# Kernel tuning notes

Hardware: AMD Instinct MI355X
Metric: run time of the kernel (lower is better)

## Reference

```python
import jax, jax.numpy as jnp
from jax import lax
import numpy as np

C = 64          # in_channel
CL = 32         # latent channels = in_channel // latent_dim
IC = 32         # inter_channel
GH, GW = 8, 8   # grid


def conv1x1(x, W, b):
    # x: [N,C,H,W], W: [O,C], b: [O]
    return jnp.einsum('nchw,oc->nohw', x, W) + b[None, :, None, None]


def maxpool2(x):
    return lax.reduce_window(x, -jnp.inf, lax.max, (1, 1, 2, 2), (1, 1, 2, 2), 'VALID')


def conv3x3(x, W, b):
    y = lax.conv_general_dilated(x, W, (1, 1), ((1, 1), (1, 1)),
                                 dimension_numbers=('NCHW', 'OIHW', 'NCHW'))
    return y + b[None, :, None, None]


def setup_inputs() -> dict:
    key = jax.random.key(0)
    ks = jax.random.split(key, 20)
    s = 0.05
    inp = {
        'x': jax.random.normal(ks[0], (4, C, 256, 256), jnp.float32),
        # Self_Attn_FM params (1x1 convs stored as matrices)
        'Wq': jax.random.normal(ks[1], (CL, C), jnp.float32) * s,
        'bq': jnp.zeros((CL,), jnp.float32),
        'Wk': jax.random.normal(ks[2], (CL, C), jnp.float32) * s,
        'bk': jnp.zeros((CL,), jnp.float32),
        'Wv': jax.random.normal(ks[3], (CL, C), jnp.float32) * s,
        'bv': jnp.zeros((CL,), jnp.float32),
        'Wo': jax.random.normal(ks[4], (C, CL), jnp.float32) * s,
        'bo': jnp.zeros((C,), jnp.float32),
        'gamma': jax.random.normal(ks[5], ()) * 0.5,
        # dense conv blocks: dims 64 -> 96 -> 128, each -> 32
        'W1': jax.random.normal(ks[6], (IC, C, 3, 3), jnp.float32) * s,
        'b1': jnp.zeros((IC,), jnp.float32),
        'W2': jax.random.normal(ks[7], (IC, C + IC, 3, 3), jnp.float32) * s,
        'b2': jnp.zeros((IC,), jnp.float32),
        'W3': jax.random.normal(ks[8], (IC, C + 2 * IC, 3, 3), jnp.float32) * s,
        'b3': jnp.zeros((IC,), jnp.float32),
        # fusion 1x1: (C + 3*IC) -> C
        'Wf': jax.random.normal(ks[9], (C, C + 3 * IC), jnp.float32) * s,
        'bf': jnp.zeros((C,), jnp.float32),
    }
    return inp


def region_non_local(x, Wq, bq, Wk, bk, Wv, bv, Wo, bo, gamma):
    B, Cc, H, W = x.shape
    h, w = H // GH, W // GW
    # split into grid cells, batched: [B*GH*GW, C, h, w]
    cells = x.reshape(B, Cc, GH, h, GW, w).transpose(0, 2, 4, 1, 3, 5)
    cells = cells.reshape(B * GH * GW, Cc, h, w)
    N, L = cells.shape[0], h * w
    q = conv1x1(cells, Wq, bq).reshape(N, CL, L)                 # [N,c,L]
    k = maxpool2(conv1x1(cells, Wk, bk)).reshape(N, CL, L // 4)  # [N,c,L/4]
    v = maxpool2(conv1x1(cells, Wv, bv)).reshape(N, CL, L // 4)
    attn = jax.nn.softmax(jnp.einsum('ncq,nck->nqk', q, k), axis=-1)
    out = jnp.einsum('nck,nqk->ncq', v, attn).reshape(N, CL, h, w)
    out = gamma * conv1x1(out, Wo, bo) + cells
    # regroup cells back to [B,C,H,W]
    out = out.reshape(B, GH, GW, Cc, h, w).transpose(0, 3, 1, 4, 2, 5)
    return out.reshape(B, Cc, H, W)


def reference(x, Wq, bq, Wk, bk, Wv, bv, Wo, bo, gamma,
              W1, b1, W2, b2, W3, b3, Wf, bf):
    f0 = region_non_local(x, Wq, bq, Wk, bk, Wv, bv, Wo, bo, gamma)
    f1 = jax.nn.relu(conv3x3(f0, W1, b1))
    f2 = jax.nn.relu(conv3x3(jnp.concatenate([f0, f1], axis=1), W2, b2))
    f3 = jax.nn.relu(conv3x3(jnp.concatenate([f0, f1, f2], axis=1), W3, b3))
    cat = jnp.concatenate([f0, f1, f2, f3], axis=1)
    out = conv1x1(cat, Wf, bf) + x
    return out
```

## Files before the change

### kernel.cpp

```cpp
#include <hip/hip_runtime.h>


typedef short s16x8 __attribute__((ext_vector_type(8)));
typedef float f32x4 __attribute__((ext_vector_type(4)));
typedef unsigned short ushort_t;

__device__ __forceinline__ unsigned short f2bf(float f) {
  union { float f; unsigned int u; } v; v.f = f;
  unsigned int r = v.u + 0x7fffu + ((v.u >> 16) & 1u);
  return (unsigned short)(r >> 16);
}
__device__ __forceinline__ float bf2f(unsigned short h) {
  union { unsigned int u; float f; } v; v.u = ((unsigned int)h) << 16;
  return v.f;
}

__global__ void repack_kernel(const float* __restrict__ W1, const float* __restrict__ W2,
                              const float* __restrict__ W3, const float* __restrict__ Wf,
                              ushort_t* __restrict__ wc1, ushort_t* __restrict__ wc2,
                              ushort_t* __restrict__ wc3, ushort_t* __restrict__ wff)
{
  const int i = blockIdx.x * 256 + threadIdx.x;
  if (i < 18432) {
    int j = i & 7, o = (i >> 3) & 31, r = i >> 8, tap = r >> 3, kg = r & 7;
    wc1[i] = f2bf(W1[o * 576 + (kg * 8 + j) * 9 + tap]);
  }
  if (i < 27648) {
    int j = i & 7, o = (i >> 3) & 31, r = i >> 8, tap = r / 12, kg = r % 12;
    wc2[i] = f2bf(W2[o * 864 + (kg * 8 + j) * 9 + tap]);
  }
  if (i < 36864) {
    int j = i & 7, o = (i >> 3) & 31, r = i >> 8, tap = r >> 4, kg = r & 15;
    wc3[i] = f2bf(W3[o * 1152 + (kg * 8 + j) * 9 + tap]);
  }
  if (i < 10240) {
    int j = i & 7, o = (i >> 3) & 63, kg = i >> 9;
    wff[i] = f2bf(Wf[o * 160 + kg * 8 + j]);
  }
}

__global__ __launch_bounds__(256, 4) void kvx_kernel(
    const float* __restrict__ x,
    const float* __restrict__ Wk, const float* __restrict__ bk,
    const float* __restrict__ Wv, const float* __restrict__ bv,
    ushort_t* __restrict__ xt, ushort_t* __restrict__ kg, ushort_t* __restrict__ vt)
{
  __shared__ ushort_t kvs[4][8][64];

  const int bid = blockIdx.x;
  const int cell = bid >> 3;
  const int tid = threadIdx.x, lane = tid & 63, wv = tid >> 6;
  const int w = (bid & 7) * 4 + wv;
  const int yp = w >> 1, h = w & 1;
  const int quad = lane >> 4, l15 = lane & 15;

  const int n  = cell >> 6;
  const int gh = (cell >> 3) & 7;
  const int gw = cell & 7;
  const int y0 = gh * 32, xc0 = gw * 32;
  const float* xn  = x  + (size_t)n * (64 * 65536);
  ushort_t*    xtn = xt + (size_t)n * (65536 * 64);

  s16x8 wkf[2][2], wvf[2][2];
#pragma unroll
  for (int ks = 0; ks < 2; ++ks)
#pragma unroll
    for (int nt = 0; nt < 2; ++nt) {
      const int off = (nt * 16 + l15) * 64 + ks * 32 + quad * 8;
      s16x8 tk, tv;
#pragma unroll
      for (int j = 0; j < 8; ++j) {
        tk[j] = (short)f2bf(Wk[off + j]);
        tv[j] = (short)f2bf(Wv[off + j]);
      }
      wkf[ks][nt] = tk; wvf[ks][nt] = tv;
    }
  float bkv[2], bvv[2];
#pragma unroll
  for (int nt = 0; nt < 2; ++nt) {
    bkv[nt] = bk[nt * 16 + l15];
    bvv[nt] = bv[nt * 16 + l15];
  }

  const f32x4 zf = {0.f, 0.f, 0.f, 0.f};
  f32x4 kd[2][2], vd[2][2];

#pragma unroll
  for (int t2 = 0; t2 < 2; ++t2) {
    const int yy = 2 * yp + t2;
    const int xx = h * 16 + l15;
    const float* px = xn + (y0 + yy) * 256 + xc0 + xx;

    s16x8 a[2];
#pragma unroll
    for (int ks = 0; ks < 2; ++ks)
#pragma unroll
      for (int j = 0; j < 8; ++j)
        a[ks][j] = (short)f2bf(px[(size_t)(ks * 32 + quad * 8 + j) * 65536]);

    const size_t pixg = (size_t)((y0 + yy) * 256 + xc0 + xx);
    *(s16x8*)(xtn + pixg * 64 + quad * 8)      = a[0];
    *(s16x8*)(xtn + pixg * 64 + 32 + quad * 8) = a[1];

#pragma unroll
    for (int nt = 0; nt < 2; ++nt) {
      kd[t2][nt] = zf; vd[t2][nt] = zf;
#pragma unroll
      for (int ks = 0; ks < 2; ++ks) {
        kd[t2][nt] = __builtin_amdgcn_mfma_f32_16x16x32_bf16(a[ks], wkf[ks][nt], kd[t2][nt], 0, 0, 0);
        vd[t2][nt] = __builtin_amdgcn_mfma_f32_16x16x32_bf16(a[ks], wvf[ks][nt], vd[t2][nt], 0, 0, 0);
      }
    }
  }

#pragma unroll
  for (int nt = 0; nt < 2; ++nt) {
#pragma unroll
    for (int r = 0; r < 2; ++r) {
      const float kp = fmaxf(fmaxf(kd[0][nt][2 * r], kd[0][nt][2 * r + 1]),
                             fmaxf(kd[1][nt][2 * r], kd[1][nt][2 * r + 1])) + bkv[nt];
      const float vp = fmaxf(fmaxf(vd[0][nt][2 * r], vd[0][nt][2 * r + 1]),
                             fmaxf(vd[1][nt][2 * r], vd[1][nt][2 * r + 1])) + bvv[nt];
      kvs[wv][quad * 2 + r][nt * 16 + l15]      = f2bf(kp);
      kvs[wv][quad * 2 + r][32 + nt * 16 + l15] = f2bf(vp);
    }
  }
  __syncthreads();

  const int kpos0 = yp * 16 + h * 8;
  if (lane < 32) {
    const s16x8 vv = *(const s16x8*)&kvs[wv][lane >> 2][(lane & 3) * 8];
    *(s16x8*)(kg + ((size_t)(cell << 8) + kpos0 + (lane >> 2)) * 32 + (lane & 3) * 8) = vv;
  } else {
    const int ch = lane - 32;
    s16x8 vv;
#pragma unroll
    for (int r = 0; r < 8; ++r) vv[r] = (short)kvs[wv][r][32 + ch];
    *(s16x8*)(vt + (size_t)(cell << 13) + ch * 256 + kpos0) = vv;
  }
}

__global__ __launch_bounds__(256, 3) void attn_kernel(
    const ushort_t* __restrict__ xt, const ushort_t* __restrict__ kg,
    const ushort_t* __restrict__ vt,
    const float* __restrict__ Wq, const float* __restrict__ bq,
    const float* __restrict__ Wo, const float* __restrict__ bo,
    const float* __restrict__ gamma_p, ushort_t* __restrict__ f0)
{
  __shared__ __attribute__((aligned(16))) ushort_t kl[256 * 36];
  __shared__ __attribute__((aligned(16))) ushort_t vl[32 * 260];
  __shared__ __attribute__((aligned(16))) ushort_t un[4][2176];

  const int bid = blockIdx.x;
  const int cell = bid >> 2;
  const int part = bid & 3;
  const int tid = threadIdx.x, lane = tid & 63, wv = tid >> 6;
  const int quad = lane >> 4, l15 = lane & 15;

  const int n  = cell >> 6;
  const int gh = (cell >> 3) & 7;
  const int gw = cell & 7;
  const int y0 = gh * 32, xc0 = gw * 32;

  const ushort_t* xtn = xt + (size_t)n * (65536 * 64);
  ushort_t*       f0n = f0 + (size_t)n * (65536 * 64);
  const ushort_t* kc  = kg + (size_t)(cell << 8) * 32;
  const ushort_t* vc  = vt + (size_t)(cell << 13);

  for (int idx = tid; idx < 1024; idx += 256) {
    const int kpos = idx >> 2, cg = idx & 3;
    *(s16x8*)&kl[kpos * 36 + cg * 8] = *(const s16x8*)(kc + kpos * 32 + cg * 8);
  }
  for (int idx = tid; idx < 1024; idx += 256) {
    const int ch = idx >> 5, seg = idx & 31;
    *(s16x8*)&vl[ch * 260 + seg * 8] = *(const s16x8*)(vc + ch * 256 + seg * 8);
  }

  const float gamma = gamma_p[0];

  s16x8 wqf[2][2];
#pragma unroll
  for (int ks = 0; ks < 2; ++ks)
#pragma unroll
    for (int nt = 0; nt < 2; ++nt) {
      const float* p = Wq + (nt * 16 + l15) * 64 + ks * 32 + quad * 8;
      s16x8 t;
#pragma unroll
      for (int j = 0; j < 8; ++j) t[j] = (short)f2bf(p[j]);
      wqf[ks][nt] = t;
    }
  s16x8 wof[4];
#pragma unroll
  for (int nt = 0; nt < 4; ++nt) {
    const float* p = Wo + (nt * 16 + l15) * 32 + quad * 8;
    s16x8 t;
#pragma unroll
    for (int j = 0; j < 8; ++j) t[j] = (short)f2bf(p[j]);
    wof[nt] = t;
  }
  float bqv[2]; bqv[0] = bq[l15]; bqv[1] = bq[16 + l15];
  float bov[4];
#pragma unroll
  for (int nt = 0; nt < 4; ++nt) bov[nt] = bo[nt * 16 + l15];

  __syncthreads();

  ushort_t* uw = un[wv];
  const f32x4 zf = {0.f, 0.f, 0.f, 0.f};

#pragma unroll 1
  for (int it = 0; it < 4; ++it) {
    const int mt = part * 16 + wv * 4 + it;
    const int pbase = mt * 16;

    const int p = pbase + l15;
    const int yy = p >> 5, xx = p & 31;
    const size_t pixg = (size_t)((y0 + yy) * 256 + xc0 + xx);

    const s16x8 a0 = *(const s16x8*)(xtn + pixg * 64 + quad * 8);
    const s16x8 a1 = *(const s16x8*)(xtn + pixg * 64 + 32 + quad * 8);
    f32x4 qd0 = zf, qd1 = zf;
    qd0 = __builtin_amdgcn_mfma_f32_16x16x32_bf16(a0, wqf[0][0], qd0, 0, 0, 0);
    qd0 = __builtin_amdgcn_mfma_f32_16x16x32_bf16(a1, wqf[1][0], qd0, 0, 0, 0);
    qd1 = __builtin_amdgcn_mfma_f32_16x16x32_bf16(a0, wqf[0][1], qd1, 0, 0, 0);
    qd1 = __builtin_amdgcn_mfma_f32_16x16x32_bf16(a1, wqf[1][1], qd1, 0, 0, 0);
#pragma unroll
    for (int i = 0; i < 4; ++i) {
      uw[(quad * 4 + i) * 40 + l15]      = f2bf(qd0[i] + bqv[0]);
      uw[(quad * 4 + i) * 40 + 16 + l15] = f2bf(qd1[i] + bqv[1]);
    }
    const s16x8 qa = *(const s16x8*)&uw[l15 * 40 + quad * 8];

    f32x4 S[16];
#pragma unroll
    for (int nt = 0; nt < 16; ++nt) {
      const s16x8 kb = *(const s16x8*)&kl[(nt * 16 + l15) * 36 + quad * 8];
      S[nt] = __builtin_amdgcn_mfma_f32_16x16x32_bf16(qa, kb, zf, 0, 0, 0);
    }

    float rl[4];
#pragma unroll
    for (int i = 0; i < 4; ++i) {
      float m = S[0][i];
#pragma unroll
      for (int nt = 1; nt < 16; ++nt) m = fmaxf(m, S[nt][i]);
#pragma unroll
      for (int d2 = 1; d2 < 16; d2 <<= 1) m = fmaxf(m, __shfl_xor(m, d2, 64));
      float s = 0.f;
#pragma unroll
      for (int nt = 0; nt < 16; ++nt) {
        float e = __expf(S[nt][i] - m);
        S[nt][i] = e;
        s += e;
      }
#pragma unroll
      for (int d2 = 1; d2 < 16; d2 <<= 1) s += __shfl_xor(s, d2, 64);
      rl[i] = s;
    }

    f32x4 O0 = zf, O1 = zf;
#pragma unroll
    for (int hh = 0; hh < 2; ++hh) {
#pragma unroll
      for (int t = 0; t < 8; ++t)
#pragma unroll
        for (int i = 0; i < 4; ++i)
          uw[(quad * 4 + i) * 136 + t * 16 + l15] = f2bf(S[hh * 8 + t][i]);
#pragma unroll
      for (int kk = 0; kk < 4; ++kk) {
        const s16x8 pa = *(const s16x8*)&uw[l15 * 136 + kk * 32 + quad * 8];
        const int kb0 = hh * 128 + kk * 32 + quad * 8;
        const s16x8 vb0 = *(const s16x8*)&vl[l15 * 260 + kb0];
        const s16x8 vb1 = *(const s16x8*)&vl[(16 + l15) * 260 + kb0];
        O0 = __builtin_amdgcn_mfma_f32_16x16x32_bf16(pa, vb0, O0, 0, 0, 0);
        O1 = __builtin_amdgcn_mfma_f32_16x16x32_bf16(pa, vb1, O1, 0, 0, 0);
      }
    }

#pragma unroll
    for (int i = 0; i < 4; ++i) {
      const float inv = 1.0f / rl[i];
      uw[(quad * 4 + i) * 40 + l15]      = f2bf(O0[i] * inv);
      uw[(quad * 4 + i) * 40 + 16 + l15] = f2bf(O1[i] * inv);
    }
    const s16x8 oa = *(const s16x8*)&uw[l15 * 40 + quad * 8];
#pragma unroll
    for (int nt = 0; nt < 4; ++nt) {
      f32x4 D = __builtin_amdgcn_mfma_f32_16x16x32_bf16(oa, wof[nt], zf, 0, 0, 0);
#pragma unroll
      for (int i = 0; i < 4; ++i)
        uw[(quad * 4 + i) * 72 + nt * 16 + l15] = f2bf(gamma * (D[i] + bov[nt]));
    }

    {
      const s16x8 fv0 = *(const s16x8*)&uw[l15 * 72 + quad * 16];
      const s16x8 fv1 = *(const s16x8*)&uw[l15 * 72 + quad * 16 + 8];
      const s16x8 xv0 = *(const s16x8*)(xtn + pixg * 64 + quad * 16);
      const s16x8 xv1 = *(const s16x8*)(xtn + pixg * 64 + quad * 16 + 8);
      s16x8 r0, r1;
#pragma unroll
      for (int j = 0; j < 8; ++j) {
        r0[j] = (short)f2bf(bf2f((unsigned short)fv0[j]) + bf2f((unsigned short)xv0[j]));
        r1[j] = (short)f2bf(bf2f((unsigned short)fv1[j]) + bf2f((unsigned short)xv1[j]));
      }
      *(s16x8*)(f0n + pixg * 64 + quad * 16)     = r0;
      *(s16x8*)(f0n + pixg * 64 + quad * 16 + 8) = r1;
    }
  }
}

template <int NCHUNK>
__global__ __launch_bounds__(256) void conv3_kernel(
    const ushort_t* __restrict__ s0, const ushort_t* __restrict__ s1,
    const ushort_t* __restrict__ s2, const ushort_t* __restrict__ wc,
    const float* __restrict__ bias, ushort_t* __restrict__ outp)
{
  __shared__ __attribute__((aligned(16))) ushort_t tile[612 * 40];

  const int bid = blockIdx.x;
  const int n = bid >> 7;
  const int t = bid & 127;
  const int ty0 = (t >> 3) * 16;
  const int tx0 = (t & 7) * 32;
  const int tid = threadIdx.x, lane = tid & 63, wv = tid >> 6;
  const int quad = lane >> 4, l15 = lane & 15;
  constexpr int Kg = NCHUNK * 4;

  const f32x4 zf = {0.f, 0.f, 0.f, 0.f};
  f32x4 acc[4][2][2];
#pragma unroll
  for (int r = 0; r < 4; ++r)
#pragma unroll
    for (int h = 0; h < 2; ++h) { acc[r][h][0] = zf; acc[r][h][1] = zf; }

  for (int ch = 0; ch < NCHUNK; ++ch) {
    const ushort_t* src; int cstr, cbase;
    if (ch < 2)       { src = s0 + (size_t)n * (65536 * 64); cstr = 64; cbase = ch * 32; }
    else if (ch == 2) { src = s1 + (size_t)n * (65536 * 32); cstr = 32; cbase = 0; }
    else              { src = s2 + (size_t)n * (65536 * 32); cstr = 32; cbase = 0; }

    __syncthreads();
    for (int u = tid; u < 2448; u += 256) {
      const int pix = u >> 2, cg = u & 3;
      const int lr = pix / 34, lc = pix - lr * 34;
      const int gy = ty0 - 1 + lr, gx = tx0 - 1 + lc;
      s16x8 v = {0, 0, 0, 0, 0, 0, 0, 0};
      if ((unsigned)gy < 256u && (unsigned)gx < 256u)
        v = *(const s16x8*)(src + (size_t)(gy * 256 + gx) * cstr + cbase + cg * 8);
      *(s16x8*)&tile[pix * 40 + cg * 8] = v;
    }
    __syncthreads();

#pragma unroll
    for (int tap = 0; tap < 9; ++tap) {
      const int ky = tap / 3, kx = tap - ky * 3;
      const ushort_t* wb = wc + ((size_t)(tap * Kg + ch * 4 + quad) * 32 + l15) * 8;
      const s16x8 b0 = *(const s16x8*)wb;
      const s16x8 b1 = *(const s16x8*)(wb + 128);
#pragma unroll
      for (int r = 0; r < 4; ++r) {
        const int lr = 4 * wv + r + ky;
#pragma unroll
        for (int h = 0; h < 2; ++h) {
          const int lc = h * 16 + l15 + kx;
          const s16x8 a = *(const s16x8*)&tile[(lr * 34 + lc) * 40 + quad * 8];
          acc[r][h][0] = __builtin_amdgcn_mfma_f32_16x16x32_bf16(a, b0, acc[r][h][0], 0, 0, 0);
          acc[r][h][1] = __builtin_amdgcn_mfma_f32_16x16x32_bf16(a, b1, acc[r][h][1], 0, 0, 0);
        }
      }
    }
  }

  const float bv0 = bias[l15], bv1 = bias[16 + l15];
  ushort_t* on = outp + (size_t)n * (65536 * 32);
#pragma unroll
  for (int r = 0; r < 4; ++r) {
    const int gy = ty0 + 4 * wv + r;
#pragma unroll
    for (int h = 0; h < 2; ++h) {
#pragma unroll
      for (int i = 0; i < 4; ++i) {
        const int gx = tx0 + h * 16 + quad * 4 + i;
        ushort_t* op = on + (size_t)(gy * 256 + gx) * 32;
        op[l15]      = f2bf(fmaxf(acc[r][h][0][i] + bv0, 0.f));
        op[16 + l15] = f2bf(fmaxf(acc[r][h][1][i] + bv1, 0.f));
      }
    }
  }
}

__global__ __launch_bounds__(256) void fuse_kernel(
    const ushort_t* __restrict__ f0, const ushort_t* __restrict__ f1,
    const ushort_t* __restrict__ f2, const ushort_t* __restrict__ f3,
    const float* __restrict__ x, const ushort_t* __restrict__ wff,
    const float* __restrict__ bfv, float* __restrict__ out)
{
  __shared__ float tr[4][64 * 17];

  const int tid = threadIdx.x, lane = tid & 63, wv = tid >> 6;
  const int quad = lane >> 4, l15 = lane & 15;

  s16x8 wf[5][4];
#pragma unroll
  for (int ks = 0; ks < 5; ++ks)
#pragma unroll
    for (int nt = 0; nt < 4; ++nt)
      wf[ks][nt] = *(const s16x8*)(wff + ((size_t)((ks * 4 + quad) * 64) + nt * 16 + l15) * 8);
  float bb[4];
#pragma unroll
  for (int nt = 0; nt < 4; ++nt) bb[nt] = bfv[nt * 16 + l15];

  const int wt = blockIdx.x * 4 + wv;
  const f32x4 zf = {0.f, 0.f, 0.f, 0.f};
  float* trw = tr[wv];

  for (int mt = 0; mt < 4; ++mt) {
    const int p0 = wt * 64 + mt * 16;
    const size_t pA = (size_t)(p0 + l15);
    const s16x8 a0 = *(const s16x8*)(f0 + pA * 64 + quad * 8);
    const s16x8 a1 = *(const s16x8*)(f0 + pA * 64 + 32 + quad * 8);
    const s16x8 a2 = *(const s16x8*)(f1 + pA * 32 + quad * 8);
    const s16x8 a3 = *(const s16x8*)(f2 + pA * 32 + quad * 8);
    const s16x8 a4 = *(const s16x8*)(f3 + pA * 32 + quad * 8);

    f32x4 acc[4];
#pragma unroll
    for (int nt = 0; nt < 4; ++nt) {
      f32x4 d = zf;
      d = __builtin_amdgcn_mfma_f32_16x16x32_bf16(a0, wf[0][nt], d, 0, 0, 0);
      d = __builtin_amdgcn_mfma_f32_16x16x32_bf16(a1, wf[1][nt], d, 0, 0, 0);
      d = __builtin_amdgcn_mfma_f32_16x16x32_bf16(a2, wf[2][nt], d, 0, 0, 0);
      d = __builtin_amdgcn_mfma_f32_16x16x32_bf16(a3, wf[3][nt], d, 0, 0, 0);
      d = __builtin_amdgcn_mfma_f32_16x16x32_bf16(a4, wf[4][nt], d, 0, 0, 0);
      acc[nt] = d;
    }

#pragma unroll
    for (int nt = 0; nt < 4; ++nt)
#pragma unroll
      for (int i = 0; i < 4; ++i)
        trw[(nt * 16 + l15) * 17 + quad * 4 + i] = acc[nt][i] + bb[nt];

    const int n = p0 >> 16;
    const int pix0 = p0 & 65535;
    const float* xb = x + (size_t)n * (64 * 65536);
    float* ob = out + (size_t)n * (64 * 65536);
#pragma unroll
    for (int og = 0; og < 16; ++og) {
      const int o = og * 4 + quad;
      const float v = trw[o * 17 + l15];
      const size_t g = (size_t)o * 65536 + pix0 + l15;
      ob[g] = v + xb[g];
    }
  }
}

extern "C" void kernel_launch(void* const* d_in, const int* in_sizes, int n_in,
                              void* d_out, int out_size, void* d_ws, size_t ws_size,
                              hipStream_t stream)
{
  const float* x     = (const float*)d_in[0];
  const float* Wq    = (const float*)d_in[1];
  const float* bq    = (const float*)d_in[2];
  const float* Wk    = (const float*)d_in[3];
  const float* bk    = (const float*)d_in[4];
  const float* Wv    = (const float*)d_in[5];
  const float* bv    = (const float*)d_in[6];
  const float* Wo    = (const float*)d_in[7];
  const float* bo    = (const float*)d_in[8];
  const float* gamma = (const float*)d_in[9];
  const float* W1    = (const float*)d_in[10];
  const float* b1    = (const float*)d_in[11];
  const float* W2    = (const float*)d_in[12];
  const float* b2    = (const float*)d_in[13];
  const float* W3    = (const float*)d_in[14];
  const float* b3    = (const float*)d_in[15];
  const float* Wf    = (const float*)d_in[16];
  const float* bf    = (const float*)d_in[17];

  float* out = (float*)d_out;
  ushort_t* wsu = (ushort_t*)d_ws;

  ushort_t* f0 = wsu;
  ushort_t* f1 = wsu + 16777216;
  ushort_t* f2 = wsu + 25165824;
  ushort_t* f3 = wsu + 33554432;
  ushort_t* xtb = wsu + 16777216;
  ushort_t* kgb = wsu + 33554432;
  ushort_t* vtb = wsu + 35651584;
  ushort_t* wc1 = wsu + 41943040;
  ushort_t* wc2 = wc1 + 18432;
  ushort_t* wc3 = wc2 + 27648;
  ushort_t* wff = wc3 + 36864;

  repack_kernel<<<144, 256, 0, stream>>>(W1, W2, W3, Wf, wc1, wc2, wc3, wff);
  kvx_kernel<<<2048, 256, 0, stream>>>(x, Wk, bk, Wv, bv, xtb, kgb, vtb);
  attn_kernel<<<1024, 256, 0, stream>>>(xtb, kgb, vtb, Wq, bq, Wo, bo, gamma, f0);
  conv3_kernel<2><<<512, 256, 0, stream>>>(f0, f1, f2, wc1, b1, f1);
  conv3_kernel<3><<<512, 256, 0, stream>>>(f0, f1, f2, wc2, b2, f2);
  conv3_kernel<4><<<512, 256, 0, stream>>>(f0, f1, f2, wc3, b3, f3);
  fuse_kernel<<<1024, 256, 0, stream>>>(f0, f1, f2, f3, x, wff, bf, out);
}
```

Measured before the change: 342.5 us.

## Stage x rows through LDS in kvx kernel for coalesced vectorized loads

Each kvx block now covers a 2-row by 128-pixel strip for one image. It loads that strip from x with coalesced float4 reads, converts to bf16 and writes it into a padded LDS tile. The channel-last xt copy and the K/V MFMA inputs are then gathered from LDS, replacing the earlier scattered per-channel global loads with a 65536 stride. The grid is halved and each wave processes two tiles, at the cost of about 33KB of LDS per block and an extra barrier, which may reduce occupancy.

```diff
diff --git a/kernel.cpp b/kernel.cpp
--- a/kernel.cpp
+++ b/kernel.cpp
@@ -45,21 +45,37 @@
     const float* __restrict__ Wv, const float* __restrict__ bv,
     ushort_t* __restrict__ xt, ushort_t* __restrict__ kg, ushort_t* __restrict__ vt)
 {
+  __shared__ __attribute__((aligned(16))) ushort_t lds[64 * 258];
   __shared__ ushort_t kvs[4][8][64];
 
   const int bid = blockIdx.x;
-  const int cell = bid >> 3;
+  const int n   = bid >> 8;
+  const int rem = bid & 255;
+  const int pr  = rem >> 1;
+  const int xh  = rem & 1;
   const int tid = threadIdx.x, lane = tid & 63, wv = tid >> 6;
-  const int w = (bid & 7) * 4 + wv;
-  const int yp = w >> 1, h = w & 1;
   const int quad = lane >> 4, l15 = lane & 15;
 
-  const int n  = cell >> 6;
-  const int gh = (cell >> 3) & 7;
-  const int gw = cell & 7;
-  const int y0 = gh * 32, xc0 = gw * 32;
-  const float* xn  = x  + (size_t)n * (64 * 65536);
-  ushort_t*    xtn = xt + (size_t)n * (65536 * 64);
+  const int y0 = pr * 2;
+  const int x0 = xh * 128;
+  const int gh = pr >> 4, pyc = pr & 15;
+
+  const float* xblk = x + (size_t)n * (64 * 65536) + (size_t)(y0 * 256 + x0);
+  ushort_t*    xtn  = xt + (size_t)n * (65536 * 64);
+
+#pragma unroll 4
+  for (int i = 0; i < 16; ++i) {
+    const int idx = (i << 8) + tid;
+    const int c  = idx >> 6;
+    const int r  = (idx >> 5) & 1;
+    const int sg = idx & 31;
+    const f32x4 v = *(const f32x4*)(xblk + (size_t)c * 65536 + r * 256 + sg * 4);
+    const unsigned int lo = (unsigned int)f2bf(v[0]) | ((unsigned int)f2bf(v[1]) << 16);
+    const unsigned int hi = (unsigned int)f2bf(v[2]) | ((unsigned int)f2bf(v[3]) << 16);
+    const int base = c * 258 + (r << 7) + (sg << 2);
+    *(unsigned int*)&lds[base]     = lo;
+    *(unsigned int*)&lds[base + 2] = hi;
+  }
 
   s16x8 wkf[2][2], wvf[2][2];
 #pragma unroll
@@ -82,61 +98,76 @@
     bvv[nt] = bv[nt * 16 + l15];
   }
 
+  __syncthreads();
+
+  {
+    const int g  = lane & 7;
+    const int pa = lane >> 3;
+#pragma unroll
+    for (int s = 0; s < 8; ++s) {
+      const int p = (wv << 6) + (s << 3) + pa;
+      s16x8 v;
+#pragma unroll
+      for (int j = 0; j < 8; ++j) v[j] = (short)lds[(g * 8 + j) * 258 + p];
+      const int P = (y0 + (p >> 7)) * 256 + x0 + (p & 127);
+      *(s16x8*)(xtn + (size_t)P * 64 + g * 8) = v;
+    }
+  }
+
   const f32x4 zf = {0.f, 0.f, 0.f, 0.f};
-  f32x4 kd[2][2], vd[2][2];
-
-#pragma unroll
-  for (int t2 = 0; t2 < 2; ++t2) {
-    const int yy = 2 * yp + t2;
-    const int xx = h * 16 + l15;
-    const float* px = xn + (y0 + yy) * 256 + xc0 + xx;
-
-    s16x8 a[2];
-#pragma unroll
-    for (int ks = 0; ks < 2; ++ks)
-#pragma unroll
-      for (int j = 0; j < 8; ++j)
-        a[ks][j] = (short)f2bf(px[(size_t)(ks * 32 + quad * 8 + j) * 65536]);
-
-    const size_t pixg = (size_t)((y0 + yy) * 256 + xc0 + xx);
-    *(s16x8*)(xtn + pixg * 64 + quad * 8)      = a[0];
-    *(s16x8*)(xtn + pixg * 64 + 32 + quad * 8) = a[1];
-
-#pragma unroll
-    for (int nt = 0; nt < 2; ++nt) {
-      kd[t2][nt] = zf; vd[t2][nt] = zf;
+#pragma unroll
+  for (int tt = 0; tt < 2; ++tt) {
+    const int t   = wv * 2 + tt;
+    const int px0 = t * 16 + l15;
+
+    s16x8 a[2][2];
+#pragma unroll
+    for (int r = 0; r < 2; ++r)
 #pragma unroll
       for (int ks = 0; ks < 2; ++ks) {
-        kd[t2][nt] = __builtin_amdgcn_mfma_f32_16x16x32_bf16(a[ks], wkf[ks][nt], kd[t2][nt], 0, 0, 0);
-        vd[t2][nt] = __builtin_amdgcn_mfma_f32_16x16x32_bf16(a[ks], wvf[ks][nt], vd[t2][nt], 0, 0, 0);
-      }
-    }
-  }
-
-#pragma unroll
-  for (int nt = 0; nt < 2; ++nt) {
-#pragma unroll
-    for (int r = 0; r < 2; ++r) {
-      const float kp = fmaxf(fmaxf(kd[0][nt][2 * r], kd[0][nt][2 * r + 1]),
-                             fmaxf(kd[1][nt][2 * r], kd[1][nt][2 * r + 1])) + bkv[nt];
-      const float vp = fmaxf(fmaxf(vd[0][nt][2 * r], vd[0][nt][2 * r + 1]),
-                             fmaxf(vd[1][nt][2 * r], vd[1][nt][2 * r + 1])) + bvv[nt];
-      kvs[wv][quad * 2 + r][nt * 16 + l15]      = f2bf(kp);
-      kvs[wv][quad * 2 + r][32 + nt * 16 + l15] = f2bf(vp);
-    }
-  }
-  __syncthreads();
-
-  const int kpos0 = yp * 16 + h * 8;
-  if (lane < 32) {
-    const s16x8 vv = *(const s16x8*)&kvs[wv][lane >> 2][(lane & 3) * 8];
-    *(s16x8*)(kg + ((size_t)(cell << 8) + kpos0 + (lane >> 2)) * 32 + (lane & 3) * 8) = vv;
-  } else {
-    const int ch = lane - 32;
-    s16x8 vv;
-#pragma unroll
-    for (int r = 0; r < 8; ++r) vv[r] = (short)kvs[wv][r][32 + ch];
-    *(s16x8*)(vt + (size_t)(cell << 13) + ch * 256 + kpos0) = vv;
+        s16x8 v;
+#pragma unroll
+        for (int j = 0; j < 8; ++j)
+          v[j] = (short)lds[(ks * 32 + quad * 8 + j) * 258 + (r << 7) + px0];
+        a[r][ks] = v;
+      }
+
+    f32x4 kd[2][2], vd[2][2];
+#pragma unroll
+    for (int r = 0; r < 2; ++r)
+#pragma unroll
+      for (int nt = 0; nt < 2; ++nt) {
+        f32x4 k0 = __builtin_amdgcn_mfma_f32_16x16x32_bf16(a[r][0], wkf[0][nt], zf, 0, 0, 0);
+        kd[r][nt] = __builtin_amdgcn_mfma_f32_16x16x32_bf16(a[r][1], wkf[1][nt], k0, 0, 0, 0);
+        f32x4 v0 = __builtin_amdgcn_mfma_f32_16x16x32_bf16(a[r][0], wvf[0][nt], zf, 0, 0, 0);
+        vd[r][nt] = __builtin_amdgcn_mfma_f32_16x16x32_bf16(a[r][1], wvf[1][nt], v0, 0, 0, 0);
+      }
+
+#pragma unroll
+    for (int nt = 0; nt < 2; ++nt)
+#pragma unroll
+      for (int rr = 0; rr < 2; ++rr) {
+        const float kp = fmaxf(fmaxf(kd[0][nt][2 * rr], kd[0][nt][2 * rr + 1]),
+                               fmaxf(kd[1][nt][2 * rr], kd[1][nt][2 * rr + 1])) + bkv[nt];
+        const float vp = fmaxf(fmaxf(vd[0][nt][2 * rr], vd[0][nt][2 * rr + 1]),
+                               fmaxf(vd[1][nt][2 * rr], vd[1][nt][2 * rr + 1])) + bvv[nt];
+        kvs[wv][quad * 2 + rr][nt * 16 + l15]      = f2bf(kp);
+        kvs[wv][quad * 2 + rr][32 + nt * 16 + l15] = f2bf(vp);
+      }
+
+    const int gw    = xh * 4 + (t >> 1);
+    const int cell  = (n << 6) + (gh << 3) + gw;
+    const int kposb = pyc * 16 + (t & 1) * 8;
+    if (lane < 32) {
+      const s16x8 vv = *(const s16x8*)&kvs[wv][lane >> 2][(lane & 3) * 8];
+      *(s16x8*)(kg + ((size_t)(cell << 8) + kposb + (lane >> 2)) * 32 + (lane & 3) * 8) = vv;
+    } else {
+      const int ch = lane - 32;
+      s16x8 vv;
+#pragma unroll
+      for (int r = 0; r < 8; ++r) vv[r] = (short)kvs[wv][r][32 + ch];
+      *(s16x8*)(vt + (size_t)(cell << 13) + ch * 256 + kposb) = vv;
+    }
   }
 }
 
@@ -494,7 +525,7 @@
   ushort_t* wff = wc3 + 36864;
 
   repack_kernel<<<144, 256, 0, stream>>>(W1, W2, W3, Wf, wc1, wc2, wc3, wff);
-  kvx_kernel<<<2048, 256, 0, stream>>>(x, Wk, bk, Wv, bv, xtb, kgb, vtb);
+  kvx_kernel<<<1024, 256, 0, stream>>>(x, Wk, bk, Wv, bv, xtb, kgb, vtb);
   attn_kernel<<<1024, 256, 0, stream>>>(xtb, kgb, vtb, Wq, bq, Wo, bo, gamma, f0);
   conv3_kernel<2><<<512, 256, 0, stream>>>(f0, f1, f2, wc1, b1, f1);
   conv3_kernel<3><<<512, 256, 0, stream>>>(f0, f1, f2, wc2, b2, f2);
```

After: 338.3 us. No clear change (-1.2%).
